# Kernel optimization log

Hardware: AMD Instinct MI355X
Metric: run time of the kernel (lower is better)

Reference implementation:

```python
import jax, jax.numpy as jnp
import numpy as np

BN_EPS = 1e-5
K = 3  # number of nearest neighbors for interpolation


def setup_inputs() -> dict:
    key = jax.random.key(0)
    ks = jax.random.split(key, 16)
    B, N1, N2 = 8, 8192, 2048
    C2, C1, H = 256, 128, 256  # in_channels, skip_channels, out_channels
    total_in = C2 + C1
    inp = {
        "xyz1": jax.random.normal(ks[0], (B, 3, N1), dtype=jnp.float32),
        "xyz2": jax.random.normal(ks[1], (B, 3, N2), dtype=jnp.float32),
        "features1": jax.random.normal(ks[2], (B, C1, N1), dtype=jnp.float32),
        "features2": jax.random.normal(ks[3], (B, C2, N2), dtype=jnp.float32),
        # SharedMLP([total_in, H, H]): two 1x1 Conv1d + BatchNorm1d (eval mode) + ReLU
        "w1": jax.random.normal(ks[4], (H, total_in), dtype=jnp.float32) * 0.05,
        "b1": jax.random.normal(ks[5], (H,), dtype=jnp.float32) * 0.01,
        "g1": 1.0 + 0.1 * jax.random.normal(ks[6], (H,), dtype=jnp.float32),
        "be1": 0.1 * jax.random.normal(ks[7], (H,), dtype=jnp.float32),
        "m1": 0.1 * jax.random.normal(ks[8], (H,), dtype=jnp.float32),
        "v1": 0.5 + jax.random.uniform(ks[9], (H,), dtype=jnp.float32),
        "w2": jax.random.normal(ks[10], (H, H), dtype=jnp.float32) * 0.05,
        "b2": jax.random.normal(ks[11], (H,), dtype=jnp.float32) * 0.01,
        "g2": 1.0 + 0.1 * jax.random.normal(ks[12], (H,), dtype=jnp.float32),
        "be2": 0.1 * jax.random.normal(ks[13], (H,), dtype=jnp.float32),
        "m2": 0.1 * jax.random.normal(ks[14], (H,), dtype=jnp.float32),
        "v2": 0.5 + jax.random.uniform(ks[15], (H,), dtype=jnp.float32),
    }
    return inp


def _conv_bn_relu(x, w, b, g, be, m, v):
    # x: [B, Cin, N], w: [Cout, Cin] (1x1 conv), BN in eval mode
    y = jnp.einsum("oc,bcn->bon", w, x) + b[None, :, None]
    y = (y - m[None, :, None]) * (g / jnp.sqrt(v + BN_EPS))[None, :, None] + be[None, :, None]
    return jax.nn.relu(y)


def reference(xyz1, xyz2, features1, features2,
              w1, b1, g1, be1, m1, v1,
              w2, b2, g2, be2, m2, v2):
    # --- squared pairwise distances [B, N1, N2] ---
    x1 = jnp.transpose(xyz1, (0, 2, 1))  # [B, N1, 3]
    x2 = jnp.transpose(xyz2, (0, 2, 1))  # [B, N2, 3]
    sq = (jnp.sum(x1 * x1, axis=-1, keepdims=True)
          + jnp.sum(x2 * x2, axis=-1)[:, None, :]
          - 2.0 * jnp.einsum("bnd,bmd->bnm", x1, x2))
    # --- k=3 nearest neighbors (smallest sq distances) ---
    neg_d, idx = jax.lax.top_k(-sq, K)          # [B, N1, K]
    dist = jnp.maximum(-neg_d, 1e-10)
    weight = 1.0 / dist
    weight = weight / jnp.sum(weight, axis=-1, keepdims=True)  # [B, N1, K]
    # --- gather neighbor features and inverse-distance interpolate ---
    feat2_t = jnp.transpose(features2, (0, 2, 1))              # [B, N2, C2]
    neighbor = jax.vmap(lambda f, i: f[i])(feat2_t, idx)       # [B, N1, K, C2]
    interp = jnp.einsum("bnkc,bnk->bnc", neighbor, weight)     # [B, N1, C2]
    interp = jnp.transpose(interp, (0, 2, 1))                  # [B, C2, N1]
    # --- concat skip features and shared MLP ---
    x = jnp.concatenate([interp, features1], axis=1)           # [B, C2+C1, N1]
    x = _conv_bn_relu(x, w1, b1, g1, be1, m1, v1)
    x = _conv_bn_relu(x, w2, b2, g2, be2, m2, v2)
    return x
```

## Files before the change

kernel.cpp:

```cpp
#include <hip/hip_runtime.h>
#include <hip/hip_bf16.h>

typedef unsigned short u16;
typedef __attribute__((ext_vector_type(4))) float f32x4;
typedef __attribute__((ext_vector_type(8))) short short8;

#define BN_EPS 1e-5f

__device__ __forceinline__ u16 f2b(float x) {
  union { float f; unsigned int u; } v; v.f = x;
  unsigned int r = (v.u + 0x7FFFu + ((v.u >> 16) & 1u)) >> 16;
  return (u16)r;
}
__device__ __forceinline__ float b2f(u16 u) {
  union { unsigned int u; float f; } v; v.u = ((unsigned int)u) << 16;
  return v.f;
}

__global__ void prep_kernel(const float* __restrict__ w1, const float* __restrict__ b1,
                            const float* __restrict__ g1, const float* __restrict__ be1,
                            const float* __restrict__ m1, const float* __restrict__ v1,
                            const float* __restrict__ w2, const float* __restrict__ b2,
                            const float* __restrict__ g2, const float* __restrict__ be2,
                            const float* __restrict__ m2, const float* __restrict__ v2,
                            u16* __restrict__ w1b, u16* __restrict__ w2b,
                            float* __restrict__ al1, float* __restrict__ bt1,
                            float* __restrict__ al2, float* __restrict__ bt2) {
  int t = threadIdx.x;
  int blk = blockIdx.x;
  if (blk < 384) {
    int id = blk * 256 + t;
    unsigned o = (unsigned)id / 384u;
    unsigned c = (unsigned)id % 384u;
    w1b[(c >> 5) * 8192 + o * 32 + (c & 31)] = f2b(w1[id]);
  } else if (blk < 640) {
    int j = (blk - 384) * 256 + t;
    unsigned o = (unsigned)j >> 8;
    unsigned c = (unsigned)j & 255u;
    w2b[(c >> 5) * 8192 + o * 32 + (c & 31)] = f2b(w2[j]);
  } else if (blk == 640) {
    float a = g1[t] / sqrtf(v1[t] + BN_EPS);
    al1[t] = a;
    bt1[t] = (b1[t] - m1[t]) * a + be1[t];
  } else {
    float a = g2[t] / sqrtf(v2[t] + BN_EPS);
    al2[t] = a;
    bt2[t] = (b2[t] - m2[t]) * a + be2[t];
  }
}

__global__ void transpose_f2_kernel(const float* __restrict__ f2, u16* __restrict__ f2t) {
  __shared__ float tile[32][33];
  int t = threadIdx.x;
  int tx = t & 31, ty = t >> 5;
  int b = blockIdx.z;
  int n2t = blockIdx.x * 32, ct = blockIdx.y * 32;
#pragma unroll
  for (int i = 0; i < 4; ++i) {
    int c = ct + ty + i * 8;
    tile[ty + i * 8][tx] = f2[((size_t)b * 256 + c) * 2048 + n2t + tx];
  }
  __syncthreads();
#pragma unroll
  for (int i = 0; i < 4; ++i) {
    int n2 = n2t + ty + i * 8;
    f2t[((size_t)b * 2048 + n2) * 256 + ct + tx] = f2b(tile[tx][ty + i * 8]);
  }
}

__global__ __launch_bounds__(256) void knn_interp_kernel(
    const float* __restrict__ xyz1, const float* __restrict__ xyz2,
    const float* __restrict__ f1, const u16* __restrict__ f2t,
    u16* __restrict__ xb) {
  union Lds {
    struct { float4 pts[2048]; float md[256 * 3]; int mi[256 * 3]; } a;
    float f1t[128 * 65];
  };
  __shared__ Lds lds;
  __shared__ float wts[64 * 3];
  __shared__ int idxs[64 * 3];

  int t = threadIdx.x;
  int b = blockIdx.x >> 7;
  int n1_0 = (blockIdx.x & 127) * 64;
  int panel = blockIdx.x;

  const float* x2 = xyz2 + b * 3 * 2048;
  for (int j = t; j < 2048; j += 256) {
    float cx = x2[j], cy = x2[2048 + j], cz = x2[4096 + j];
    float nsq = (cx * cx + cy * cy) + cz * cz;
    lds.a.pts[j] = make_float4(cx, cy, cz, nsq);
  }
  __syncthreads();

  {
    int p = t & 63, s = t >> 6;
    int n1 = n1_0 + p;
    const float* x1 = xyz1 + b * 3 * 8192;
    float bx = x1[n1], by = x1[8192 + n1], bz = x1[16384 + n1];
    float n1sq = (bx * bx + by * by) + bz * bz;
    float nx = -2.f * bx, ny = -2.f * by, nz = -2.f * bz;
    float d0 = 3.4e38f, d1 = 3.4e38f, d2 = 3.4e38f;
    int i0 = 0, i1 = 0, i2 = 0;
    int jb = s * 512;
#pragma unroll 4
    for (int jj = 0; jj < 512; ++jj) {
      float4 c = lds.a.pts[jb + jj];
      float sq = fmaf(nx, c.x, fmaf(ny, c.y, fmaf(nz, c.z, n1sq + c.w)));
      int j = jb + jj;
      bool c0 = sq < d0, c1 = sq < d1, c2 = sq < d2;
      d2 = c1 ? d1 : (c2 ? sq : d2);  i2 = c1 ? i1 : (c2 ? j : i2);
      d1 = c0 ? d0 : (c1 ? sq : d1); i1 = c0 ? i0 : (c1 ? j : i1);
      d0 = c0 ? sq : d0;             i0 = c0 ? j : i0;
    }
    lds.a.md[t * 3 + 0] = d0; lds.a.md[t * 3 + 1] = d1; lds.a.md[t * 3 + 2] = d2;
    lds.a.mi[t * 3 + 0] = i0; lds.a.mi[t * 3 + 1] = i1; lds.a.mi[t * 3 + 2] = i2;
  }
  __syncthreads();
  if (t < 64) {
    float d0 = 3.4e38f, d1 = 3.4e38f, d2 = 3.4e38f;
    int i0 = 0, i1 = 0, i2 = 0;
#pragma unroll
    for (int s = 0; s < 4; ++s) {
#pragma unroll
      for (int k = 0; k < 3; ++k) {
        float d = lds.a.md[(s * 64 + t) * 3 + k];
        int i = lds.a.mi[(s * 64 + t) * 3 + k];
        bool c0 = d < d0, c1 = d < d1, c2 = d < d2;
        d2 = c1 ? d1 : (c2 ? d : d2);  i2 = c1 ? i1 : (c2 ? i : i2);
        d1 = c0 ? d0 : (c1 ? d : d1); i1 = c0 ? i0 : (c1 ? i : i1);
        d0 = c0 ? d : d0;             i0 = c0 ? i : i0;
      }
    }
    float e0 = fmaxf(d0, 1e-10f), e1 = fmaxf(d1, 1e-10f), e2 = fmaxf(d2, 1e-10f);
    float w0 = 1.0f / e0, w1 = 1.0f / e1, w2 = 1.0f / e2;
    float sm = (w0 + w1) + w2;
    wts[t * 3 + 0] = w0 / sm; wts[t * 3 + 1] = w1 / sm; wts[t * 3 + 2] = w2 / sm;
    idxs[t * 3 + 0] = i0 * 256; idxs[t * 3 + 1] = i1 * 256; idxs[t * 3 + 2] = i2 * 256;
  }
  __syncthreads();

  {
    const u16* f2tb = f2t + (size_t)b * 2048 * 256;
    size_t xbase = (size_t)panel * 24576 + (size_t)((t >> 5) * 2048) + (t & 31);
#pragma unroll 4
    for (int p = 0; p < 64; ++p) {
      int j0 = idxs[p * 3 + 0], j1 = idxs[p * 3 + 1], j2 = idxs[p * 3 + 2];
      float w0 = wts[p * 3 + 0], w1 = wts[p * 3 + 1], w2 = wts[p * 3 + 2];
      float v = (w0 * b2f(f2tb[j0 + t]) + w1 * b2f(f2tb[j1 + t]))
                + w2 * b2f(f2tb[j2 + t]);
      xb[xbase + p * 32] = f2b(v);
    }
  }
  __syncthreads();

  {
    const float* f1b = f1 + (size_t)b * 128 * 8192 + n1_0;
    for (int it = 0; it < 32; ++it) {
      int c = it * 4 + (t >> 6);
      int n = t & 63;
      lds.f1t[c * 65 + n] = f1b[(size_t)c * 8192 + n];
    }
    __syncthreads();
    for (int it = 0; it < 32; ++it) {
      int v = it * 256 + t;
      int c = v & 127, p = v >> 7;
      float val = lds.f1t[c * 65 + p];
      xb[(size_t)panel * 24576 + (size_t)(8 + (c >> 5)) * 2048 + p * 32 + (c & 31)] = f2b(val);
    }
  }
}

template <int KT, bool FINAL>
__global__ __launch_bounds__(256, 3) void gemm_kernel(
    const u16* __restrict__ xin, const u16* __restrict__ wb,
    const float* __restrict__ alpha, const float* __restrict__ beta,
    u16* __restrict__ yout, float* __restrict__ fout) {
  int t = threadIdx.x;
  int panel = blockIdx.x;
  int w = t >> 6, lane = t & 63, l15 = lane & 15, quad = lane >> 4;

  f32x4 acc[4][4];
#pragma unroll
  for (int m = 0; m < 4; ++m)
#pragma unroll
    for (int n = 0; n < 4; ++n)
      acc[m][n] = (f32x4){0.f, 0.f, 0.f, 0.f};

  const u16* aw = wb + (size_t)(w * 64 + l15) * 32 + quad * 8;
  const u16* bx = xin + (size_t)panel * (KT * 2048) + (size_t)l15 * 32 + quad * 8;

#pragma unroll 2
  for (int kt = 0; kt < KT; ++kt) {
    short8 af[4], bf[4];
#pragma unroll
    for (int m = 0; m < 4; ++m)
      af[m] = *(const short8*)(aw + kt * 8192 + m * 512);
#pragma unroll
    for (int n = 0; n < 4; ++n)
      bf[n] = *(const short8*)(bx + kt * 2048 + n * 512);
#pragma unroll
    for (int m = 0; m < 4; ++m)
#pragma unroll
      for (int n = 0; n < 4; ++n)
        acc[m][n] = __builtin_amdgcn_mfma_f32_16x16x32_bf16(af[m], bf[n], acc[m][n], 0, 0, 0);
  }

  float al[4][4], bt[4][4];
#pragma unroll
  for (int m = 0; m < 4; ++m)
#pragma unroll
    for (int r = 0; r < 4; ++r) {
      int o = w * 64 + m * 16 + quad * 4 + r;
      al[m][r] = alpha[o];
      bt[m][r] = beta[o];
    }

  if (FINAL) {
#pragma unroll
    for (int m = 0; m < 4; ++m)
#pragma unroll
      for (int n = 0; n < 4; ++n)
#pragma unroll
        for (int r = 0; r < 4; ++r) {
          int o = w * 64 + m * 16 + quad * 4 + r;
          int col = n * 16 + l15;
          int bn = panel * 64 + col;
          int bb = bn >> 13, n1 = bn & 8191;
          float vv = fmaxf(fmaf(al[m][r], acc[m][n][r], bt[m][r]), 0.f);
          fout[(size_t)(bb * 256 + o) * 8192 + n1] = vv;
        }
  } else {
    u16* yp = yout + (size_t)panel * 16384;
#pragma unroll
    for (int m = 0; m < 4; ++m)
#pragma unroll
      for (int n = 0; n < 4; ++n) {
        int col = n * 16 + l15;
        ushort4 pk;
        pk.x = f2b(fmaxf(fmaf(al[m][0], acc[m][n][0], bt[m][0]), 0.f));
        pk.y = f2b(fmaxf(fmaf(al[m][1], acc[m][n][1], bt[m][1]), 0.f));
        pk.z = f2b(fmaxf(fmaf(al[m][2], acc[m][n][2], bt[m][2]), 0.f));
        pk.w = f2b(fmaxf(fmaf(al[m][3], acc[m][n][3], bt[m][3]), 0.f));
        *(ushort4*)(yp + (size_t)(w * 2 + (m >> 1)) * 2048 + col * 32 +
                    (m & 1) * 16 + quad * 4) = pk;
      }
  }
}

extern "C" void kernel_launch(void* const* d_in, const int* in_sizes, int n_in,
                              void* d_out, int out_size, void* d_ws, size_t ws_size,
                              hipStream_t stream) {
  const float* xyz1 = (const float*)d_in[0];
  const float* xyz2 = (const float*)d_in[1];
  const float* f1   = (const float*)d_in[2];
  const float* f2   = (const float*)d_in[3];
  const float* w1   = (const float*)d_in[4];
  const float* b1   = (const float*)d_in[5];
  const float* g1   = (const float*)d_in[6];
  const float* be1  = (const float*)d_in[7];
  const float* m1   = (const float*)d_in[8];
  const float* v1   = (const float*)d_in[9];
  const float* w2   = (const float*)d_in[10];
  const float* b2   = (const float*)d_in[11];
  const float* g2   = (const float*)d_in[12];
  const float* be2  = (const float*)d_in[13];
  const float* m2   = (const float*)d_in[14];
  const float* v2   = (const float*)d_in[15];

  char* ws = (char*)d_ws;
  u16* xb   = (u16*)(ws);
  u16* y1   = (u16*)(ws + 50331648);
  u16* f2t  = (u16*)(ws + 50331648);
  u16* w1b  = (u16*)(ws + 83886080);
  u16* w2b  = (u16*)(ws + 84082688);
  float* al1 = (float*)(ws + 84213760);
  float* bt1 = (float*)(ws + 84214784);
  float* al2 = (float*)(ws + 84215808);
  float* bt2 = (float*)(ws + 84216832);
  float* out = (float*)d_out;

  prep_kernel<<<642, 256, 0, stream>>>(w1, b1, g1, be1, m1, v1,
                                       w2, b2, g2, be2, m2, v2,
                                       w1b, w2b, al1, bt1, al2, bt2);
  transpose_f2_kernel<<<dim3(64, 8, 8), 256, 0, stream>>>(f2, f2t);
  knn_interp_kernel<<<1024, 256, 0, stream>>>(xyz1, xyz2, f1, f2t, xb);
  gemm_kernel<12, false><<<1024, 256, 0, stream>>>(xb, w1b, al1, bt1, y1, nullptr);
  gemm_kernel<8, true><<<1024, 256, 0, stream>>>(y1, w2b, al2, bt2, nullptr, out);
}
```

Baseline: 248.8 us.

## Process 128 points per KNN block and stage GEMM epilogues through LDS

The KNN kernel now handles 128 query points per block, with each thread tracking 4 queries. Every candidate point loaded from LDS is therefore reused four times, and the top-3 distance update uses min/max instead of selects. Both GEMM epilogues now stage their results in dynamic shared memory so the global writes become coalesced vector stores, notably the strided fp32 output. This adds LDS usage, which led to lowering the GEMM occupancy hint from 3 to 2, and gives the KNN kernel fewer blocks and higher register pressure.

```diff
diff --git a/kernel.cpp b/kernel.cpp
--- a/kernel.cpp
+++ b/kernel.cpp
@@ -73,17 +73,17 @@
     const float* __restrict__ f1, const u16* __restrict__ f2t,
     u16* __restrict__ xb) {
   union Lds {
-    struct { float4 pts[2048]; float md[256 * 3]; int mi[256 * 3]; } a;
-    float f1t[128 * 65];
+    struct { float4 pts[2048]; float md[8 * 128 * 3]; int mi[8 * 128 * 3]; } a;
+    float f1t[128 * 129];
   };
   __shared__ Lds lds;
-  __shared__ float wts[64 * 3];
-  __shared__ int idxs[64 * 3];
+  __shared__ float wts[128 * 3];
+  __shared__ int idxs[128 * 3];
 
   int t = threadIdx.x;
-  int b = blockIdx.x >> 7;
-  int n1_0 = (blockIdx.x & 127) * 64;
-  int panel = blockIdx.x;
+  int b = blockIdx.x >> 6;
+  int n1_0 = (blockIdx.x & 63) * 128;
+  int panel0 = blockIdx.x * 2;
 
   const float* x2 = xyz2 + b * 3 * 2048;
   for (int j = t; j < 2048; j += 256) {
@@ -94,42 +94,64 @@
   __syncthreads();
 
   {
-    int p = t & 63, s = t >> 6;
-    int n1 = n1_0 + p;
+    int qg = t & 31, s = t >> 5;
     const float* x1 = xyz1 + b * 3 * 8192;
-    float bx = x1[n1], by = x1[8192 + n1], bz = x1[16384 + n1];
-    float n1sq = (bx * bx + by * by) + bz * bz;
-    float nx = -2.f * bx, ny = -2.f * by, nz = -2.f * bz;
+    float nx[4], ny[4], nz[4], nsq1[4];
+    float d[4][3];
+    int id[4][3];
+#pragma unroll
+    for (int i = 0; i < 4; ++i) {
+      int n1 = n1_0 + qg + 32 * i;
+      float bx = x1[n1], by = x1[8192 + n1], bz = x1[16384 + n1];
+      nsq1[i] = (bx * bx + by * by) + bz * bz;
+      nx[i] = -2.f * bx; ny[i] = -2.f * by; nz[i] = -2.f * bz;
+      d[i][0] = d[i][1] = d[i][2] = 3.4e38f;
+      id[i][0] = id[i][1] = id[i][2] = 0;
+    }
+    int jb = s * 256;
+#pragma unroll 4
+    for (int jj = 0; jj < 256; ++jj) {
+      float4 c = lds.a.pts[jb + jj];
+      int j = jb + jj;
+#pragma unroll
+      for (int i = 0; i < 4; ++i) {
+        float sq = fmaf(nx[i], c.x, fmaf(ny[i], c.y, fmaf(nz[i], c.z, nsq1[i] + c.w)));
+        bool c0 = sq < d[i][0], c1 = sq < d[i][1], c2 = sq < d[i][2];
+        id[i][2] = c1 ? id[i][1] : (c2 ? j : id[i][2]);
+        id[i][1] = c0 ? id[i][0] : (c1 ? j : id[i][1]);
+        id[i][0] = c0 ? j : id[i][0];
+        d[i][2] = fminf(fmaxf(sq, d[i][1]), d[i][2]);
+        d[i][1] = fminf(fmaxf(sq, d[i][0]), d[i][1]);
+        d[i][0] = fminf(sq, d[i][0]);
+      }
+    }
+#pragma unroll
+    for (int i = 0; i < 4; ++i) {
+      int q = qg + 32 * i;
+#pragma unroll
+      for (int k = 0; k < 3; ++k) {
+        lds.a.md[(s * 128 + q) * 3 + k] = d[i][k];
+        lds.a.mi[(s * 128 + q) * 3 + k] = id[i][k];
+      }
+    }
+  }
+  __syncthreads();
+  if (t < 128) {
     float d0 = 3.4e38f, d1 = 3.4e38f, d2 = 3.4e38f;
     int i0 = 0, i1 = 0, i2 = 0;
-    int jb = s * 512;
-#pragma unroll 4
-    for (int jj = 0; jj < 512; ++jj) {
-      float4 c = lds.a.pts[jb + jj];
-      float sq = fmaf(nx, c.x, fmaf(ny, c.y, fmaf(nz, c.z, n1sq + c.w)));
-      int j = jb + jj;
-      bool c0 = sq < d0, c1 = sq < d1, c2 = sq < d2;
-      d2 = c1 ? d1 : (c2 ? sq : d2);  i2 = c1 ? i1 : (c2 ? j : i2);
-      d1 = c0 ? d0 : (c1 ? sq : d1); i1 = c0 ? i0 : (c1 ? j : i1);
-      d0 = c0 ? sq : d0;             i0 = c0 ? j : i0;
-    }
-    lds.a.md[t * 3 + 0] = d0; lds.a.md[t * 3 + 1] = d1; lds.a.md[t * 3 + 2] = d2;
-    lds.a.mi[t * 3 + 0] = i0; lds.a.mi[t * 3 + 1] = i1; lds.a.mi[t * 3 + 2] = i2;
-  }
-  __syncthreads();
-  if (t < 64) {
-    float d0 = 3.4e38f, d1 = 3.4e38f, d2 = 3.4e38f;
-    int i0 = 0, i1 = 0, i2 = 0;
-#pragma unroll
-    for (int s = 0; s < 4; ++s) {
+#pragma unroll
+    for (int s = 0; s < 8; ++s) {
 #pragma unroll
       for (int k = 0; k < 3; ++k) {
-        float d = lds.a.md[(s * 64 + t) * 3 + k];
-        int i = lds.a.mi[(s * 64 + t) * 3 + k];
-        bool c0 = d < d0, c1 = d < d1, c2 = d < d2;
-        d2 = c1 ? d1 : (c2 ? d : d2);  i2 = c1 ? i1 : (c2 ? i : i2);
-        d1 = c0 ? d0 : (c1 ? d : d1); i1 = c0 ? i0 : (c1 ? i : i1);
-        d0 = c0 ? d : d0;             i0 = c0 ? i : i0;
+        float dd = lds.a.md[(s * 128 + t) * 3 + k];
+        int ii = lds.a.mi[(s * 128 + t) * 3 + k];
+        bool c0 = dd < d0, c1 = dd < d1, c2 = dd < d2;
+        i2 = c1 ? i1 : (c2 ? ii : i2);
+        i1 = c0 ? i0 : (c1 ? ii : i1);
+        i0 = c0 ? ii : i0;
+        d2 = fminf(fmaxf(dd, d1), d2);
+        d1 = fminf(fmaxf(dd, d0), d1);
+        d0 = fminf(dd, d0);
       }
     }
     float e0 = fmaxf(d0, 1e-10f), e1 = fmaxf(d1, 1e-10f), e2 = fmaxf(d2, 1e-10f);
@@ -142,40 +164,44 @@
 
   {
     const u16* f2tb = f2t + (size_t)b * 2048 * 256;
-    size_t xbase = (size_t)panel * 24576 + (size_t)((t >> 5) * 2048) + (t & 31);
 #pragma unroll 4
-    for (int p = 0; p < 64; ++p) {
+    for (int p = 0; p < 128; ++p) {
       int j0 = idxs[p * 3 + 0], j1 = idxs[p * 3 + 1], j2 = idxs[p * 3 + 2];
       float w0 = wts[p * 3 + 0], w1 = wts[p * 3 + 1], w2 = wts[p * 3 + 2];
       float v = (w0 * b2f(f2tb[j0 + t]) + w1 * b2f(f2tb[j1 + t]))
                 + w2 * b2f(f2tb[j2 + t]);
-      xb[xbase + p * 32] = f2b(v);
+      xb[(size_t)(panel0 + (p >> 6)) * 24576 + (size_t)((t >> 5) * 2048) +
+         (p & 63) * 32 + (t & 31)] = f2b(v);
     }
   }
   __syncthreads();
 
   {
     const float* f1b = f1 + (size_t)b * 128 * 8192 + n1_0;
-    for (int it = 0; it < 32; ++it) {
-      int c = it * 4 + (t >> 6);
-      int n = t & 63;
-      lds.f1t[c * 65 + n] = f1b[(size_t)c * 8192 + n];
+#pragma unroll 2
+    for (int it = 0; it < 64; ++it) {
+      int c = it * 2 + (t >> 7);
+      int n = t & 127;
+      lds.f1t[c * 129 + n] = f1b[(size_t)c * 8192 + n];
     }
     __syncthreads();
-    for (int it = 0; it < 32; ++it) {
+#pragma unroll 2
+    for (int it = 0; it < 64; ++it) {
       int v = it * 256 + t;
       int c = v & 127, p = v >> 7;
-      float val = lds.f1t[c * 65 + p];
-      xb[(size_t)panel * 24576 + (size_t)(8 + (c >> 5)) * 2048 + p * 32 + (c & 31)] = f2b(val);
+      float val = lds.f1t[c * 129 + p];
+      xb[(size_t)(panel0 + (p >> 6)) * 24576 + (size_t)(8 + (c >> 5)) * 2048 +
+         (p & 63) * 32 + (c & 31)] = f2b(val);
     }
   }
 }
 
 template <int KT, bool FINAL>
-__global__ __launch_bounds__(256, 3) void gemm_kernel(
+__global__ __launch_bounds__(256, 2) void gemm_kernel(
     const u16* __restrict__ xin, const u16* __restrict__ wb,
     const float* __restrict__ alpha, const float* __restrict__ beta,
     u16* __restrict__ yout, float* __restrict__ fout) {
+  extern __shared__ char elraw[];
   int t = threadIdx.x;
   int panel = blockIdx.x;
   int w = t >> 6, lane = t & 63, l15 = lane & 15, quad = lane >> 4;
@@ -217,23 +243,32 @@
     }
 
   if (FINAL) {
+    float* Y2 = (float*)elraw + w * (64 * 68);
 #pragma unroll
     for (int m = 0; m < 4; ++m)
 #pragma unroll
       for (int n = 0; n < 4; ++n)
 #pragma unroll
         for (int r = 0; r < 4; ++r) {
-          int o = w * 64 + m * 16 + quad * 4 + r;
+          int ol = m * 16 + quad * 4 + r;
           int col = n * 16 + l15;
-          int bn = panel * 64 + col;
-          int bb = bn >> 13, n1 = bn & 8191;
-          float vv = fmaxf(fmaf(al[m][r], acc[m][n][r], bt[m][r]), 0.f);
-          fout[(size_t)(bb * 256 + o) * 8192 + n1] = vv;
+          Y2[ol * 68 + col] = fmaxf(fmaf(al[m][r], acc[m][n][r], bt[m][r]), 0.f);
         }
+    __syncthreads();
+    size_t obase = (size_t)(panel >> 7) * 2097152 + (size_t)((panel * 64) & 8191);
+#pragma unroll
+    for (int it = 0; it < 16; ++it) {
+      int row = it * 4 + quad;
+      int o = w * 64 + row;
+      float4 vv = *(const float4*)&Y2[row * 68 + l15 * 4];
+      *(float4*)(fout + obase + (size_t)o * 8192 + l15 * 4) = vv;
+    }
   } else {
-    u16* yp = yout + (size_t)panel * 16384;
-#pragma unroll
-    for (int m = 0; m < 4; ++m)
+    u16* Y = (u16*)elraw;
+#pragma unroll
+    for (int m = 0; m < 4; ++m) {
+      int rowbase = (w * 2 + (m >> 1)) * 64;
+      int osub = (m & 1) * 16 + quad * 4;
 #pragma unroll
       for (int n = 0; n < 4; ++n) {
         int col = n * 16 + l15;
@@ -242,9 +277,17 @@
         pk.y = f2b(fmaxf(fmaf(al[m][1], acc[m][n][1], bt[m][1]), 0.f));
         pk.z = f2b(fmaxf(fmaf(al[m][2], acc[m][n][2], bt[m][2]), 0.f));
         pk.w = f2b(fmaxf(fmaf(al[m][3], acc[m][n][3], bt[m][3]), 0.f));
-        *(ushort4*)(yp + (size_t)(w * 2 + (m >> 1)) * 2048 + col * 32 +
-                    (m & 1) * 16 + quad * 4) = pk;
+        *(ushort4*)&Y[(rowbase + col) * 40 + osub] = pk;
       }
+    }
+    __syncthreads();
+    u16* yp = yout + (size_t)panel * 16384;
+#pragma unroll
+    for (int i = 0; i < 8; ++i) {
+      int c2 = i * 256 + t;
+      int row = c2 >> 2, part = c2 & 3;
+      *(uint4*)(yp + row * 32 + part * 8) = *(const uint4*)&Y[row * 40 + part * 8];
+    }
   }
 }
 
@@ -284,7 +327,7 @@
                                        w2, b2, g2, be2, m2, v2,
                                        w1b, w2b, al1, bt1, al2, bt2);
   transpose_f2_kernel<<<dim3(64, 8, 8), 256, 0, stream>>>(f2, f2t);
-  knn_interp_kernel<<<1024, 256, 0, stream>>>(xyz1, xyz2, f1, f2t, xb);
-  gemm_kernel<12, false><<<1024, 256, 0, stream>>>(xb, w1b, al1, bt1, y1, nullptr);
-  gemm_kernel<8, true><<<1024, 256, 0, stream>>>(y1, w2b, al2, bt2, nullptr, out);
-}
+  knn_interp_kernel<<<512, 256, 0, stream>>>(xyz1, xyz2, f1, f2t, xb);
+  gemm_kernel<12, false><<<1024, 256, 512 * 40 * 2, stream>>>(xb, w1b, al1, bt1, y1, nullptr);
+  gemm_kernel<8, true><<<1024, 256, 4 * 64 * 68 * 4, stream>>>(y1, w2b, al2, bt2, nullptr, out);
+}
```

Result: slower. 297.1 us (+19.4%).
